# Optimization experiments

Measured on AMD Instinct MI355X. Metric: run time of the kernel, lower is better.

Reference implementation:

```python
import jax, jax.numpy as jnp
import numpy as np

B, C, R, E = 8192, 32, 24, 128
NUM_LOC = 100000
NUM_INNER = 200000   # inner_node_embed has NUM_INNER+1 rows; row 0 is padding_idx
NUM_SLICES = 24


def setup_inputs() -> dict:
    key = jax.random.key(0)
    ks = jax.random.split(key, 7)
    context = jax.random.randint(ks[0], (B, C), 0, NUM_LOC)
    route = jax.random.randint(ks[1], (B, R), 0, NUM_INNER + 1)
    lr = jax.random.randint(ks[2], (B, R), 0, 2)
    slice_idx = jax.random.randint(ks[3], (B,), 0, NUM_SLICES)
    input_embed = jax.random.normal(ks[4], (NUM_LOC, E), dtype=jnp.float32)
    inner_node_embed = jax.random.normal(ks[5], (NUM_INNER + 1, E), dtype=jnp.float32).at[0].set(0.0)
    slice_node_embed = jax.random.uniform(ks[6], (NUM_SLICES, E), dtype=jnp.float32)
    return {
        "context": context, "route": route, "lr": lr, "slice_idx": slice_idx,
        "input_embed": input_embed, "inner_node_embed": inner_node_embed,
        "slice_node_embed": slice_node_embed,
    }


def reference(context, route, lr, slice_idx, input_embed, inner_node_embed, slice_node_embed):
    # context embedding: gather + sum over context window -> (B, E)
    ctx = input_embed[context].sum(axis=1)
    # slice prediction: (B, num_slices) softmax, gather target slice prob -> (B,)
    slice_logits = jnp.einsum('se,be->bs', slice_node_embed, ctx)
    slice_prob = jax.nn.softmax(slice_logits, axis=1)
    slice_pre = jnp.take_along_axis(slice_prob, slice_idx[:, None], axis=1)[:, 0]
    # route scores: (B, R)
    dot = jnp.einsum('bre,be->br', inner_node_embed[route], ctx)
    lr_pre = jax.nn.sigmoid(dot)
    # (2p)^lr - p  -> p if lr==1, (1-p) if lr==0
    route_hidden = jnp.power(2.0 * lr_pre, lr.astype(lr_pre.dtype)) - lr_pre
    # padded route positions (route id == 0) contribute factor 1
    route_hidden = jnp.where(route == 0, jnp.ones((), lr_pre.dtype), route_hidden)
    # per-level product loop collapsed into a single prod over route dim
    pr_route = slice_pre * jnp.prod(route_hidden, axis=1)
    return 1.0 - pr_route.mean()
```

## Files before the change

### kernel.cpp

```cpp
#include <hip/hip_runtime.h>

#define BATCH    8192
#define CTX      32
#define ROUTES   24
#define EDIM     128
#define NSLICE   24
#define WPB      4
#define NBLOCKS  (BATCH / WPB)

__global__ __launch_bounds__(256, 8) void tale_fused(
    const int* __restrict__ context,
    const int* __restrict__ route,
    const int* __restrict__ lr,
    const int* __restrict__ slice_idx,
    const float* __restrict__ input_embed,
    const float* __restrict__ inner_node_embed,
    const float* __restrict__ slice_node_embed,
    float* __restrict__ out)
{
    const int tid  = threadIdx.x;
    const int lane = tid & 63;
    const int half = lane >> 5;
    const int sub  = lane & 31;
    const int w    = tid >> 6;
    const int b    = blockIdx.x * WPB + w;

    __shared__ float bs[WPB];

    int cidx = 0, ridx = 0, lridx = 0;
    if (lane < CTX) cidx = context[b * CTX + lane];
    if (lane < ROUTES) {
        ridx  = route[b * ROUTES + lane];
        lridx = lr[b * ROUTES + lane];
    }
    const int si = slice_idx[b];

    float4 acc = make_float4(0.f, 0.f, 0.f, 0.f);
    #pragma unroll
    for (int i = 0; i < 16; ++i) {
        const int idx = __shfl(cidx, i + (half << 4));
        const float4 v = *reinterpret_cast<const float4*>(
            input_embed + (size_t)idx * EDIM + (sub << 2));
        acc.x += v.x; acc.y += v.y; acc.z += v.z; acc.w += v.w;
    }
    acc.x += __shfl_xor(acc.x, 32);
    acc.y += __shfl_xor(acc.y, 32);
    acc.z += __shfl_xor(acc.z, 32);
    acc.w += __shfl_xor(acc.w, 32);

    float prodv = 1.f;
    #pragma unroll
    for (int i = 0; i < 12; ++i) {
        const int d   = 2 * i + half;
        const int idx = __shfl(ridx, d);
        const int l   = __shfl(lridx, d);
        const float4 v = *reinterpret_cast<const float4*>(
            inner_node_embed + (size_t)idx * EDIM + (sub << 2));
        float p = v.x * acc.x + v.y * acc.y + v.z * acc.z + v.w * acc.w;
        p += __shfl_xor(p, 16);
        p += __shfl_xor(p, 8);
        p += __shfl_xor(p, 4);
        p += __shfl_xor(p, 2);
        p += __shfl_xor(p, 1);
        const float sg = 1.f / (1.f + __expf(-p));
        float h = l ? sg : (1.f - sg);
        if (idx == 0) h = 1.f;
        prodv *= h;
    }
    prodv *= __shfl_xor(prodv, 32);

    float m = -3.0e38f, den = 0.f, selv = 0.f;
    #pragma unroll
    for (int i = 0; i < 12; ++i) {
        const int s = 2 * i + half;
        const float4 v = *reinterpret_cast<const float4*>(
            slice_node_embed + s * EDIM + (sub << 2));
        float p = v.x * acc.x + v.y * acc.y + v.z * acc.z + v.w * acc.w;
        p += __shfl_xor(p, 16);
        p += __shfl_xor(p, 8);
        p += __shfl_xor(p, 4);
        p += __shfl_xor(p, 2);
        p += __shfl_xor(p, 1);
        const float mN = fmaxf(m, p);
        den = den * __expf(m - mN) + __expf(p - mN);
        m = mN;
        if (s == si) selv = p;
    }
    const float m_o   = __shfl_xor(m, 32);
    const float den_o = __shfl_xor(den, 32);
    const float M     = fmaxf(m, m_o);
    const float dtot  = den * __expf(m - M) + den_o * __expf(m_o - M);
    const float sel   = __shfl(selv, (si & 1) << 5);
    const float slice_pre = __expf(sel - M) / dtot;

    const float pr = slice_pre * prodv;

    if (lane == 0) bs[w] = pr;
    __syncthreads();
    if (tid == 0) {
        const float s = bs[0] + bs[1] + bs[2] + bs[3];
        atomicAdd(out, 1.0f / NBLOCKS - s * (1.0f / BATCH));
    }
}

extern "C" void kernel_launch(void* const* d_in, const int* in_sizes, int n_in,
                              void* d_out, int out_size, void* d_ws, size_t ws_size,
                              hipStream_t stream)
{
    const int*   context          = (const int*)  d_in[0];
    const int*   route            = (const int*)  d_in[1];
    const int*   lr               = (const int*)  d_in[2];
    const int*   slice_idx        = (const int*)  d_in[3];
    const float* input_embed      = (const float*)d_in[4];
    const float* inner_node_embed = (const float*)d_in[5];
    const float* slice_node_embed = (const float*)d_in[6];
    float* out = (float*)d_out;

    hipMemsetAsync(out, 0, sizeof(float), stream);

    tale_fused<<<NBLOCKS, 64 * WPB, 0, stream>>>(
        context, route, lr, slice_idx,
        input_embed, inner_node_embed, slice_node_embed, out);
}
```

Baseline: 205.3 us.

## Use whole-wave float2 gathers with packed butterfly reduction of all dot products

Each wave now has all 64 lanes read float2 slices of every embedding row, rather than two half-waves reading float4 slices of different rows. This removes the cross-half context accumulation. The 24 route dot products and 24 slice logits are reduced together with a packed butterfly transpose-reduction, so each lane ends up holding one full dot product. That replaces 24 separate 5-step shuffle chains per set, and sigmoid, product and softmax are then done by wave-wide shuffles. The cost is more registers for the p/q arrays (launch bounds lowered to 4 blocks per CU), and route and context indices are now read per element as uniform loads.

New measurement: 202.8 us. Within noise of the previous version (-1.2%).

```diff
diff --git a/kernel.cpp b/kernel.cpp
--- a/kernel.cpp
+++ b/kernel.cpp
@@ -8,7 +8,41 @@
 #define WPB      4
 #define NBLOCKS  (BATCH / WPB)
 
-__global__ __launch_bounds__(256, 8) void tale_fused(
+__device__ __forceinline__ float packed_sum24(const float (&p)[24], const int lane)
+{
+    float c[12];
+    #pragma unroll
+    for (int i = 0; i < 12; ++i) {
+        const float e0 = p[2*i]   + __shfl_xor(p[2*i],   32);
+        const float e1 = p[2*i+1] + __shfl_xor(p[2*i+1], 32);
+        c[i] = (lane & 32) ? e1 : e0;
+    }
+    float d[6];
+    #pragma unroll
+    for (int i = 0; i < 6; ++i) {
+        const float e0 = c[2*i]   + __shfl_xor(c[2*i],   16);
+        const float e1 = c[2*i+1] + __shfl_xor(c[2*i+1], 16);
+        d[i] = (lane & 16) ? e1 : e0;
+    }
+    float e[3];
+    #pragma unroll
+    for (int i = 0; i < 3; ++i) {
+        const float e0 = d[2*i]   + __shfl_xor(d[2*i],   8);
+        const float e1 = d[2*i+1] + __shfl_xor(d[2*i+1], 8);
+        e[i] = (lane & 8) ? e1 : e0;
+    }
+    const float f0a = e[0] + __shfl_xor(e[0], 4);
+    const float f0b = e[1] + __shfl_xor(e[1], 4);
+    const float f0  = (lane & 4) ? f0b : f0a;
+    const float f1  = (lane & 4) ? 0.f : (e[2] + __shfl_xor(e[2], 4));
+    const float g0 = f0 + __shfl_xor(f0, 2);
+    const float g1 = f1 + __shfl_xor(f1, 2);
+    float g = (lane & 2) ? g1 : g0;
+    g += __shfl_xor(g, 1);
+    return g;
+}
+
+__global__ __launch_bounds__(256, 4) void tale_fused(
     const int* __restrict__ context,
     const int* __restrict__ route,
     const int* __restrict__ lr,
@@ -20,85 +54,97 @@
 {
     const int tid  = threadIdx.x;
     const int lane = tid & 63;
-    const int half = lane >> 5;
-    const int sub  = lane & 31;
     const int w    = tid >> 6;
-    const int b    = blockIdx.x * WPB + w;
+    const int b    = __builtin_amdgcn_readfirstlane(blockIdx.x * WPB + w);
 
     __shared__ float bs[WPB];
 
-    int cidx = 0, ridx = 0, lridx = 0;
-    if (lane < CTX) cidx = context[b * CTX + lane];
-    if (lane < ROUTES) {
-        ridx  = route[b * ROUTES + lane];
-        lridx = lr[b * ROUTES + lane];
-    }
+    const int voff = lane << 1;
+
+    const int v = ((lane >> 5) & 1) | (((lane >> 4) & 1) << 1) |
+                  (((lane >> 3) & 1) << 2) | (((lane >> 2) & 1) << 3) |
+                  (((lane >> 1) & 1) << 4);
+    const bool vvalid = (v < ROUTES);
+    const int  vcl    = vvalid ? v : 0;
+
+    const int rv = route[b * ROUTES + vcl];
+    const int lv = lr[b * ROUTES + vcl];
     const int si = slice_idx[b];
 
-    float4 acc = make_float4(0.f, 0.f, 0.f, 0.f);
+    float a0x=0.f,a0y=0.f,a1x=0.f,a1y=0.f,a2x=0.f,a2y=0.f,a3x=0.f,a3y=0.f;
     #pragma unroll
-    for (int i = 0; i < 16; ++i) {
-        const int idx = __shfl(cidx, i + (half << 4));
-        const float4 v = *reinterpret_cast<const float4*>(
-            input_embed + (size_t)idx * EDIM + (sub << 2));
-        acc.x += v.x; acc.y += v.y; acc.z += v.z; acc.w += v.w;
+    for (int i = 0; i < CTX; i += 4) {
+        const int i0 = context[b * CTX + i + 0];
+        const int i1 = context[b * CTX + i + 1];
+        const int i2 = context[b * CTX + i + 2];
+        const int i3 = context[b * CTX + i + 3];
+        const float2 r0 = *reinterpret_cast<const float2*>(input_embed + (size_t)i0 * EDIM + voff);
+        const float2 r1 = *reinterpret_cast<const float2*>(input_embed + (size_t)i1 * EDIM + voff);
+        const float2 r2 = *reinterpret_cast<const float2*>(input_embed + (size_t)i2 * EDIM + voff);
+        const float2 r3 = *reinterpret_cast<const float2*>(input_embed + (size_t)i3 * EDIM + voff);
+        a0x += r0.x; a0y += r0.y;
+        a1x += r1.x; a1y += r1.y;
+        a2x += r2.x; a2y += r2.y;
+        a3x += r3.x; a3y += r3.y;
     }
-    acc.x += __shfl_xor(acc.x, 32);
-    acc.y += __shfl_xor(acc.y, 32);
-    acc.z += __shfl_xor(acc.z, 32);
-    acc.w += __shfl_xor(acc.w, 32);
+    const float ax = (a0x + a1x) + (a2x + a3x);
+    const float ay = (a0y + a1y) + (a2y + a3y);
 
-    float prodv = 1.f;
+    float p[24];
     #pragma unroll
-    for (int i = 0; i < 12; ++i) {
-        const int d   = 2 * i + half;
-        const int idx = __shfl(ridx, d);
-        const int l   = __shfl(lridx, d);
-        const float4 v = *reinterpret_cast<const float4*>(
-            inner_node_embed + (size_t)idx * EDIM + (sub << 2));
-        float p = v.x * acc.x + v.y * acc.y + v.z * acc.z + v.w * acc.w;
-        p += __shfl_xor(p, 16);
-        p += __shfl_xor(p, 8);
-        p += __shfl_xor(p, 4);
-        p += __shfl_xor(p, 2);
-        p += __shfl_xor(p, 1);
-        const float sg = 1.f / (1.f + __expf(-p));
-        float h = l ? sg : (1.f - sg);
-        if (idx == 0) h = 1.f;
-        prodv *= h;
+    for (int r = 0; r < ROUTES; ++r) {
+        const int idx = route[b * ROUTES + r];
+        const float2 t = *reinterpret_cast<const float2*>(
+            inner_node_embed + (size_t)idx * EDIM + voff);
+        p[r] = t.x * ax + t.y * ay;
     }
-    prodv *= __shfl_xor(prodv, 32);
+    const float dotv = packed_sum24(p, lane);
 
-    float m = -3.0e38f, den = 0.f, selv = 0.f;
+    float q[24];
     #pragma unroll
-    for (int i = 0; i < 12; ++i) {
-        const int s = 2 * i + half;
-        const float4 v = *reinterpret_cast<const float4*>(
-            slice_node_embed + s * EDIM + (sub << 2));
-        float p = v.x * acc.x + v.y * acc.y + v.z * acc.z + v.w * acc.w;
-        p += __shfl_xor(p, 16);
-        p += __shfl_xor(p, 8);
-        p += __shfl_xor(p, 4);
-        p += __shfl_xor(p, 2);
-        p += __shfl_xor(p, 1);
-        const float mN = fmaxf(m, p);
-        den = den * __expf(m - mN) + __expf(p - mN);
-        m = mN;
-        if (s == si) selv = p;
+    for (int s = 0; s < NSLICE; ++s) {
+        const float2 t = *reinterpret_cast<const float2*>(
+            slice_node_embed + s * EDIM + voff);
+        q[s] = t.x * ax + t.y * ay;
     }
-    const float m_o   = __shfl_xor(m, 32);
-    const float den_o = __shfl_xor(den, 32);
-    const float M     = fmaxf(m, m_o);
-    const float dtot  = den * __expf(m - M) + den_o * __expf(m_o - M);
-    const float sel   = __shfl(selv, (si & 1) << 5);
-    const float slice_pre = __expf(sel - M) / dtot;
+    const float logv = packed_sum24(q, lane);
 
-    const float pr = slice_pre * prodv;
+    const float sg = 1.f / (1.f + __expf(-dotv));
+    float h = lv ? sg : (1.f - sg);
+    if (!vvalid || rv == 0 || (lane & 1)) h = 1.f;
+    h *= __shfl_xor(h, 32);
+    h *= __shfl_xor(h, 16);
+    h *= __shfl_xor(h, 8);
+    h *= __shfl_xor(h, 4);
+    h *= __shfl_xor(h, 2);
+    h *= __shfl_xor(h, 1);
+    const float prodv = h;
+
+    float ml = vvalid ? logv : -3.0e38f;
+    ml = fmaxf(ml, __shfl_xor(ml, 32));
+    ml = fmaxf(ml, __shfl_xor(ml, 16));
+    ml = fmaxf(ml, __shfl_xor(ml, 8));
+    ml = fmaxf(ml, __shfl_xor(ml, 4));
+    ml = fmaxf(ml, __shfl_xor(ml, 2));
+    ml = fmaxf(ml, __shfl_xor(ml, 1));
+    float ev = (vvalid && !(lane & 1)) ? __expf(logv - ml) : 0.f;
+    float den = ev;
+    den += __shfl_xor(den, 32);
+    den += __shfl_xor(den, 16);
+    den += __shfl_xor(den, 8);
+    den += __shfl_xor(den, 4);
+    den += __shfl_xor(den, 2);
+    den += __shfl_xor(den, 1);
+    const int lsel = (((si >> 4) & 1) << 1) | (((si >> 3) & 1) << 2) |
+                     (((si >> 2) & 1) << 3) | (((si >> 1) & 1) << 4) |
+                     ((si & 1) << 5);
+    const float esel = __shfl(ev, lsel);
+    const float pr = (esel / den) * prodv;
 
     if (lane == 0) bs[w] = pr;
     __syncthreads();
     if (tid == 0) {
-        const float s = bs[0] + bs[1] + bs[2] + bs[3];
+        const float s = (bs[0] + bs[1]) + (bs[2] + bs[3]);
         atomicAdd(out, 1.0f / NBLOCKS - s * (1.0f / BATCH));
     }
 }
```
